# Kernel optimization log

Hardware: AMD Instinct MI355X
Metric: run time of the kernel (lower is better)

Reference implementation:

```python
import jax, jax.numpy as jnp
import numpy as np

H, W, D = 160, 160, 16
VOXEL_SIZE = 0.4
VOL_MIN = np.array([-32.0, -32.0, -1.0], dtype=np.float32)
SCALE_MULTIPLIER = 3.0
N_GAUSS = 8192
CHUNK = 64


def setup_inputs() -> dict:
    key = jax.random.key(0)
    k1, k2, k3, k4, k5 = jax.random.split(key, 5)
    vol_min = jnp.asarray(VOL_MIN)
    vol_ext = jnp.array([64.0, 64.0, 6.4], dtype=jnp.float32)
    means3d = jax.random.uniform(k1, (N_GAUSS, 3), jnp.float32) * vol_ext + vol_min
    opacities = jax.random.uniform(k2, (N_GAUSS, 1), jnp.float32)
    # per-axis std devs: 0.2..0.8 m so 3-sigma footprint spans a handful of voxels
    scales = 0.2 + 0.6 * jax.random.uniform(k3, (N_GAUSS, 3), jnp.float32)
    rotations = jax.random.normal(k4, (N_GAUSS, 4), jnp.float32)
    features = jax.random.normal(k5, (N_GAUSS, 32), jnp.float32)
    return {"means3d": means3d, "opacities": opacities, "scales": scales,
            "rotations": rotations, "features": features}


def quat_to_rotmat(q):
    # q: [N,4] wxyz, normalized
    w, x, y, z = q[:, 0], q[:, 1], q[:, 2], q[:, 3]
    R = jnp.stack([
        jnp.stack([1 - 2 * (y * y + z * z), 2 * (x * y - w * z), 2 * (x * z + w * y)], -1),
        jnp.stack([2 * (x * y + w * z), 1 - 2 * (x * x + z * z), 2 * (y * z - w * x)], -1),
        jnp.stack([2 * (x * z - w * y), 2 * (y * z + w * x), 1 - 2 * (x * x + y * y)], -1),
    ], axis=-2)  # [N,3,3]
    return R


def _grid_coords():
    ii, jj, kk = jnp.meshgrid(jnp.arange(H), jnp.arange(W), jnp.arange(D), indexing="ij")
    idx = jnp.stack([ii, jj, kk], axis=-1).astype(jnp.float32)
    return (idx + 0.5) * VOXEL_SIZE + jnp.asarray(VOL_MIN)  # [H,W,D,3] voxel centers


def reference(means3d, opacities, scales, rotations, features):
    x = _grid_coords().reshape(-1, 3)  # [V,3]
    q = rotations / jnp.linalg.norm(rotations, axis=-1, keepdims=True)
    R = quat_to_rotmat(q)
    # covariance = R diag(s^2) R^T
    cov = jnp.einsum("nij,nj,nkj->nik", R, scales * scales, R)
    cov_inv = jnp.linalg.inv(cov)
    sigma = jnp.sqrt(jnp.diagonal(cov, axis1=1, axis2=2))  # [N,3]
    opac = opacities[:, 0]  # [N]
    n = means3d.shape[0]
    nchunks = n // CHUNK

    def chunked(a):
        return a.reshape(nchunks, CHUNK, *a.shape[1:])

    def step(acc, c):
        mu, op, sg, ci, ft = c
        diff = x[:, None, :] - mu[None, :, :]  # [V,CHUNK,3]
        maha = jnp.einsum("vci,cij,vcj->vc", diff, ci, diff)
        # local aggregation cutoff: within scale_multiplier * sigma box around mean
        mask = jnp.all(jnp.abs(diff) <= SCALE_MULTIPLIER * sg[None, :, :], axis=-1)
        w = op[None, :] * jnp.exp(-0.5 * maha) * mask  # [V,CHUNK]
        return acc + w @ ft, None

    acc0 = jnp.zeros((x.shape[0], features.shape[-1]), jnp.float32)
    xs = (chunked(means3d), chunked(opac), chunked(sigma), chunked(cov_inv), chunked(features))
    acc, _ = jax.lax.scan(step, acc0, xs)
    return acc.reshape(H, W, D, features.shape[-1])
```

## Files before the change

kernel.cpp:

```cpp
#include <hip/hip_runtime.h>

#define HH 160
#define WW 160
#define DD 16
#define NG 8192
#define VOXEL 0.4f

#define FTX 40
#define FTY 40
#define FTZ 4
#define NFT (FTX * FTY * FTZ)
#define CAP 128

#define TTX 20
#define TTY 20
#define TTZ 4


__global__ __launch_bounds__(64) void gv_precompute_bin(
    const float* __restrict__ means, const float* __restrict__ opac,
    const float* __restrict__ scales, const float* __restrict__ rots,
    float4* __restrict__ pack, int* __restrict__ tileCnt,
    int* __restrict__ tileList) {
  int g = blockIdx.x * 64 + threadIdx.x;
  if (g >= NG) return;
  float qw = rots[g * 4 + 0], qx = rots[g * 4 + 1];
  float qy = rots[g * 4 + 2], qz = rots[g * 4 + 3];
  float inv = rsqrtf(qw * qw + qx * qx + qy * qy + qz * qz);
  qw *= inv; qx *= inv; qy *= inv; qz *= inv;
  float R[3][3];
  R[0][0] = 1.f - 2.f * (qy * qy + qz * qz);
  R[0][1] = 2.f * (qx * qy - qw * qz);
  R[0][2] = 2.f * (qx * qz + qw * qy);
  R[1][0] = 2.f * (qx * qy + qw * qz);
  R[1][1] = 1.f - 2.f * (qx * qx + qz * qz);
  R[1][2] = 2.f * (qy * qz - qw * qx);
  R[2][0] = 2.f * (qx * qz - qw * qy);
  R[2][1] = 2.f * (qy * qz + qw * qx);
  R[2][2] = 1.f - 2.f * (qx * qx + qy * qy);
  float sx = scales[g * 3 + 0], sy = scales[g * 3 + 1], sz = scales[g * 3 + 2];
  float s2[3] = {sx * sx, sy * sy, sz * sz};
  float is2[3] = {1.f / s2[0], 1.f / s2[1], 1.f / s2[2]};
  float cov00 = 0.f, cov11 = 0.f, cov22 = 0.f;
  float ci00 = 0.f, ci01 = 0.f, ci02 = 0.f, ci11 = 0.f, ci12 = 0.f, ci22 = 0.f;
#pragma unroll
  for (int c = 0; c < 3; c++) {
    cov00 += R[0][c] * R[0][c] * s2[c];
    cov11 += R[1][c] * R[1][c] * s2[c];
    cov22 += R[2][c] * R[2][c] * s2[c];
    ci00 += R[0][c] * R[0][c] * is2[c];
    ci01 += R[0][c] * R[1][c] * is2[c];
    ci02 += R[0][c] * R[2][c] * is2[c];
    ci11 += R[1][c] * R[1][c] * is2[c];
    ci12 += R[1][c] * R[2][c] * is2[c];
    ci22 += R[2][c] * R[2][c] * is2[c];
  }
  float mx = means[g * 3 + 0], my = means[g * 3 + 1], mz = means[g * 3 + 2];
  float bx = 3.f * sqrtf(cov00), by = 3.f * sqrtf(cov11), bz = 3.f * sqrtf(cov22);
  float4* p = pack + (size_t)g * 4;
  p[0] = make_float4(mx, my, mz, opac[g]);
  p[1] = make_float4(bx, by, bz, ci00);
  p[2] = make_float4(ci01, ci02, ci11, ci12);
  p[3] = make_float4(ci22, 0.f, 0.f, 0.f);

  const float eps = 1e-4f;
  int i0 = (int)ceilf((mx - bx + 32.f) * 2.5f - 0.5f - eps);
  int i1 = (int)floorf((mx + bx + 32.f) * 2.5f - 0.5f + eps);
  int j0 = (int)ceilf((my - by + 32.f) * 2.5f - 0.5f - eps);
  int j1 = (int)floorf((my + by + 32.f) * 2.5f - 0.5f + eps);
  int k0 = (int)ceilf((mz - bz + 1.f) * 2.5f - 0.5f - eps);
  int k1 = (int)floorf((mz + bz + 1.f) * 2.5f - 0.5f + eps);
  i0 = max(i0, 0); i1 = min(i1, HH - 1);
  j0 = max(j0, 0); j1 = min(j1, WW - 1);
  k0 = max(k0, 0); k1 = min(k1, DD - 1);
  if (i0 > i1 || j0 > j1 || k0 > k1) return;
  int ti0 = i0 >> 2, ti1 = i1 >> 2;
  int tj0 = j0 >> 2, tj1 = j1 >> 2;
  int tk0 = k0 >> 2, tk1 = k1 >> 2;
  for (int ti = ti0; ti <= ti1; ti++)
    for (int tj = tj0; tj <= tj1; tj++)
      for (int tk = tk0; tk <= tk1; tk++) {
        int t = (ti * FTY + tj) * FTZ + tk;
        int pos = atomicAdd(&tileCnt[t], 1);
        if (pos < CAP) tileList[t * CAP + pos] = g;
      }
}

__global__ __launch_bounds__(256) void gv_voxelize(
    const float4* __restrict__ pack, const float4* __restrict__ feats,
    const int* __restrict__ tileCnt, const int* __restrict__ tileList,
    float4* __restrict__ out) {
  int tid = threadIdx.x;
  int w = tid >> 6;
  int wi = w >> 1, wj = w & 1;
  int l = tid & 63;
  int dk = l & 3, dj = wj * 4 + ((l >> 2) & 3), di = wi * 4 + (l >> 4);
  int tk = blockIdx.x, tj = blockIdx.y, ti = blockIdx.z;
  int i = ti * 8 + di, j = tj * 8 + dj, k = tk * 4 + dk;

  float px = (i + 0.5f) * VOXEL - 32.f;
  float py = (j + 0.5f) * VOXEL - 32.f;
  float pz = (k + 0.5f) * VOXEL - 1.f;

  int sti = ti * 2 + wi, stj = tj * 2 + wj, stk = tk;
  int t = __builtin_amdgcn_readfirstlane((sti * FTY + stj) * FTZ + stk);
  int cnt = __builtin_amdgcn_readfirstlane(tileCnt[t]);
  cnt = min(cnt, CAP);
  const int* __restrict__ lst = tileList + t * CAP;

  float4 acc[8];
#pragma unroll
  for (int f = 0; f < 8; f++) acc[f] = make_float4(0.f, 0.f, 0.f, 0.f);

  int n = 0;
  for (; n + 2 <= cnt; n += 2) {
    int g0 = __builtin_amdgcn_readfirstlane(lst[n]);
    int g1 = __builtin_amdgcn_readfirstlane(lst[n + 1]);
    const float4* __restrict__ p0 = pack + (size_t)g0 * 4;
    const float4* __restrict__ p1 = pack + (size_t)g1 * 4;
    float4 a0 = p0[0], b0 = p0[1], c0 = p0[2], d0 = p0[3];
    float4 a1 = p1[0], b1 = p1[1], c1 = p1[2], d1 = p1[3];

    float dx0 = px - a0.x, dy0 = py - a0.y, dz0 = pz - a0.z;
    float dx1 = px - a1.x, dy1 = py - a1.y, dz1 = pz - a1.z;
    bool in0 = (fabsf(dx0) <= b0.x) & (fabsf(dy0) <= b0.y) & (fabsf(dz0) <= b0.z);
    bool in1 = (fabsf(dx1) <= b1.x) & (fabsf(dy1) <= b1.y) & (fabsf(dz1) <= b1.z);

    if (__any(in0)) {
      float maha = b0.w * dx0 * dx0 + c0.z * dy0 * dy0 + d0.x * dz0 * dz0 +
                   2.f * (c0.x * dx0 * dy0 + c0.y * dx0 * dz0 + c0.w * dy0 * dz0);
      float wgt = in0 ? a0.w * __expf(-0.5f * maha) : 0.f;
      const float4* __restrict__ fp = feats + (size_t)g0 * 8;
#pragma unroll
      for (int f = 0; f < 8; f++) {
        float4 fv = fp[f];
        acc[f].x += wgt * fv.x;
        acc[f].y += wgt * fv.y;
        acc[f].z += wgt * fv.z;
        acc[f].w += wgt * fv.w;
      }
    }
    if (__any(in1)) {
      float maha = b1.w * dx1 * dx1 + c1.z * dy1 * dy1 + d1.x * dz1 * dz1 +
                   2.f * (c1.x * dx1 * dy1 + c1.y * dx1 * dz1 + c1.w * dy1 * dz1);
      float wgt = in1 ? a1.w * __expf(-0.5f * maha) : 0.f;
      const float4* __restrict__ fp = feats + (size_t)g1 * 8;
#pragma unroll
      for (int f = 0; f < 8; f++) {
        float4 fv = fp[f];
        acc[f].x += wgt * fv.x;
        acc[f].y += wgt * fv.y;
        acc[f].z += wgt * fv.z;
        acc[f].w += wgt * fv.w;
      }
    }
  }
  if (n < cnt) {
    int gg = __builtin_amdgcn_readfirstlane(lst[n]);
    const float4* __restrict__ p = pack + (size_t)gg * 4;
    float4 pa = p[0], pb = p[1];
    float dx = px - pa.x, dy = py - pa.y, dz = pz - pa.z;
    bool in = (fabsf(dx) <= pb.x) & (fabsf(dy) <= pb.y) & (fabsf(dz) <= pb.z);
    if (__any(in)) {
      float4 pc = p[2], pd = p[3];
      float maha = pb.w * dx * dx + pc.z * dy * dy + pd.x * dz * dz +
                   2.f * (pc.x * dx * dy + pc.y * dx * dz + pc.w * dy * dz);
      float wgt = in ? pa.w * __expf(-0.5f * maha) : 0.f;
      const float4* __restrict__ fp = feats + (size_t)gg * 8;
#pragma unroll
      for (int f = 0; f < 8; f++) {
        float4 fv = fp[f];
        acc[f].x += wgt * fv.x;
        acc[f].y += wgt * fv.y;
        acc[f].z += wgt * fv.z;
        acc[f].w += wgt * fv.w;
      }
    }
  }

  size_t v = ((size_t)i * WW + j) * DD + k;
  float4* o = out + v * 8;
#pragma unroll
  for (int f = 0; f < 8; f++) o[f] = acc[f];
}

extern "C" void kernel_launch(void* const* d_in, const int* in_sizes, int n_in,
                              void* d_out, int out_size, void* d_ws, size_t ws_size,
                              hipStream_t stream) {
  const float* means  = (const float*)d_in[0];
  const float* opac   = (const float*)d_in[1];
  const float* scales = (const float*)d_in[2];
  const float* rots   = (const float*)d_in[3];
  const float4* feats = (const float4*)d_in[4];

  char* ws = (char*)d_ws;
  float4* pack   = (float4*)ws;
  int* tileCnt   = (int*)(ws + 512 * 1024);
  int* tileList  = (int*)(ws + 544 * 1024);

  hipMemsetAsync(tileCnt, 0, NFT * sizeof(int), stream);
  gv_precompute_bin<<<128, 64, 0, stream>>>(means, opac, scales, rots,
                                            pack, tileCnt, tileList);
  dim3 grid(TTZ, TTY, TTX);
  gv_voxelize<<<grid, 256, 0, stream>>>(pack, feats, tileCnt, tileList,
                                        (float4*)d_out);
}
```

Baseline: 131.7 us.

## Bin per 8x8x4 block tile and software-prefetch next Gaussian pair

Gaussians are now binned to coarse 8x8x4 tiles matching the voxelize block, replacing the per-wave 4x4x4 sub-tiles, with list capacity raised to 256. The whole block shares one list. The main loop also prefetches the next pair's index and packed parameters before computing the current pair, hiding load latency. The trade is that each wave now tests Gaussians that may not touch its own sub-tile, which means more wasted iterations, and that the tile count is no longer forced scalar with readfirstlane.

```diff
diff --git a/kernel.cpp b/kernel.cpp
--- a/kernel.cpp
+++ b/kernel.cpp
@@ -6,15 +6,11 @@
 #define NG 8192
 #define VOXEL 0.4f
 
-#define FTX 40
-#define FTY 40
-#define FTZ 4
-#define NFT (FTX * FTY * FTZ)
-#define CAP 128
-
 #define TTX 20
 #define TTY 20
 #define TTZ 4
+#define NTILES (TTX * TTY * TTZ)
+#define CAP 256
 
 
 __global__ __launch_bounds__(64) void gv_precompute_bin(
@@ -74,13 +70,13 @@
   j0 = max(j0, 0); j1 = min(j1, WW - 1);
   k0 = max(k0, 0); k1 = min(k1, DD - 1);
   if (i0 > i1 || j0 > j1 || k0 > k1) return;
-  int ti0 = i0 >> 2, ti1 = i1 >> 2;
-  int tj0 = j0 >> 2, tj1 = j1 >> 2;
+  int ti0 = i0 >> 3, ti1 = i1 >> 3;
+  int tj0 = j0 >> 3, tj1 = j1 >> 3;
   int tk0 = k0 >> 2, tk1 = k1 >> 2;
   for (int ti = ti0; ti <= ti1; ti++)
     for (int tj = tj0; tj <= tj1; tj++)
       for (int tk = tk0; tk <= tk1; tk++) {
-        int t = (ti * FTY + tj) * FTZ + tk;
+        int t = (ti * TTY + tj) * TTZ + tk;
         int pos = atomicAdd(&tileCnt[t], 1);
         if (pos < CAP) tileList[t * CAP + pos] = g;
       }
@@ -91,10 +87,7 @@
     const int* __restrict__ tileCnt, const int* __restrict__ tileList,
     float4* __restrict__ out) {
   int tid = threadIdx.x;
-  int w = tid >> 6;
-  int wi = w >> 1, wj = w & 1;
-  int l = tid & 63;
-  int dk = l & 3, dj = wj * 4 + ((l >> 2) & 3), di = wi * 4 + (l >> 4);
+  int dk = tid & 3, dj = (tid >> 2) & 7, di = tid >> 5;
   int tk = blockIdx.x, tj = blockIdx.y, ti = blockIdx.z;
   int i = ti * 8 + di, j = tj * 8 + dj, k = tk * 4 + dk;
 
@@ -102,9 +95,8 @@
   float py = (j + 0.5f) * VOXEL - 32.f;
   float pz = (k + 0.5f) * VOXEL - 1.f;
 
-  int sti = ti * 2 + wi, stj = tj * 2 + wj, stk = tk;
-  int t = __builtin_amdgcn_readfirstlane((sti * FTY + stj) * FTZ + stk);
-  int cnt = __builtin_amdgcn_readfirstlane(tileCnt[t]);
+  int t = (ti * TTY + tj) * TTZ + tk;
+  int cnt = tileCnt[t];
   cnt = min(cnt, CAP);
   const int* __restrict__ lst = tileList + t * CAP;
 
@@ -112,14 +104,31 @@
 #pragma unroll
   for (int f = 0; f < 8; f++) acc[f] = make_float4(0.f, 0.f, 0.f, 0.f);
 
+  int ng0 = 0, ng1 = 0;
+  float4 A0, B0, C0, D0, A1, B1, C1, D1;
+  if (cnt >= 2) {
+    ng0 = __builtin_amdgcn_readfirstlane(lst[0]);
+    ng1 = __builtin_amdgcn_readfirstlane(lst[1]);
+    const float4* __restrict__ q0 = pack + (size_t)ng0 * 4;
+    const float4* __restrict__ q1 = pack + (size_t)ng1 * 4;
+    A0 = q0[0]; B0 = q0[1]; C0 = q0[2]; D0 = q0[3];
+    A1 = q1[0]; B1 = q1[1]; C1 = q1[2]; D1 = q1[3];
+  }
+
   int n = 0;
   for (; n + 2 <= cnt; n += 2) {
-    int g0 = __builtin_amdgcn_readfirstlane(lst[n]);
-    int g1 = __builtin_amdgcn_readfirstlane(lst[n + 1]);
-    const float4* __restrict__ p0 = pack + (size_t)g0 * 4;
-    const float4* __restrict__ p1 = pack + (size_t)g1 * 4;
-    float4 a0 = p0[0], b0 = p0[1], c0 = p0[2], d0 = p0[3];
-    float4 a1 = p1[0], b1 = p1[1], c1 = p1[2], d1 = p1[3];
+    int g0 = ng0, g1 = ng1;
+    float4 a0 = A0, b0 = B0, c0 = C0, d0 = D0;
+    float4 a1 = A1, b1 = B1, c1 = C1, d1 = D1;
+
+    if (n + 4 <= cnt) {
+      ng0 = __builtin_amdgcn_readfirstlane(lst[n + 2]);
+      ng1 = __builtin_amdgcn_readfirstlane(lst[n + 3]);
+      const float4* __restrict__ q0 = pack + (size_t)ng0 * 4;
+      const float4* __restrict__ q1 = pack + (size_t)ng1 * 4;
+      A0 = q0[0]; B0 = q0[1]; C0 = q0[2]; D0 = q0[3];
+      A1 = q1[0]; B1 = q1[1]; C1 = q1[2]; D1 = q1[3];
+    }
 
     float dx0 = px - a0.x, dy0 = py - a0.y, dz0 = pz - a0.z;
     float dx1 = px - a1.x, dy1 = py - a1.y, dz1 = pz - a1.z;
@@ -196,9 +205,9 @@
   char* ws = (char*)d_ws;
   float4* pack   = (float4*)ws;
   int* tileCnt   = (int*)(ws + 512 * 1024);
-  int* tileList  = (int*)(ws + 544 * 1024);
-
-  hipMemsetAsync(tileCnt, 0, NFT * sizeof(int), stream);
+  int* tileList  = (int*)(ws + 520 * 1024);
+
+  hipMemsetAsync(tileCnt, 0, NTILES * sizeof(int), stream);
   gv_precompute_bin<<<128, 64, 0, stream>>>(means, opac, scales, rots,
                                             pack, tileCnt, tileList);
   dim3 grid(TTZ, TTY, TTX);
```

New measurement: 131.4 us. Within noise of the previous version (-0.2%).
